# Performance work log

Hardware: AMD Instinct MI355X
Metric: run time of the kernel (lower is better)

Reference implementation:

```python
import jax, jax.numpy as jnp
import numpy as np

B, TY, TX, TT, H, VS, VT = 32, 64, 64, 64, 512, 32000, 32000


def setup_inputs() -> dict:
    key = jax.random.key(0)
    ks = jax.random.split(key, 12)
    s = 0.05  # weight scale for numerical sanity
    return {
        "y_hidden": jax.random.normal(ks[0], (B, TY, H), jnp.float32),
        "y_hidden_null": jax.random.normal(ks[1], (1, H), jnp.float32),
        "target_state": jax.random.normal(ks[2], (B, TT, H), jnp.float32),
        "W_em": jax.random.normal(ks[3], (H, H), jnp.float32) * s,
        "b_em": jnp.zeros((H,), jnp.float32),
        "W_sv": jax.random.normal(ks[4], (H, VS), jnp.float32) * s,
        "b_sv": jnp.zeros((VS,), jnp.float32),
        "W_tv": jax.random.normal(ks[5], (H, VT), jnp.float32) * s,
        "b_tv": jnp.zeros((VT,), jnp.float32),
        "sources": jax.random.randint(ks[6], (B, TX), 0, VS, jnp.int32),
        "targets": jax.random.randint(ks[7], (B, TT), 0, VT, jnp.int32),
        "target_lengths": jax.random.randint(ks[8], (B,), 1, TT + 1, jnp.int32),
    }


def reference(y_hidden, y_hidden_null, target_state, W_em, b_em, W_sv, b_sv,
              W_tv, b_tv, sources, targets, target_lengths):
    # ---- emission (get_emission) ----
    ts = jnp.tanh(y_hidden @ W_em + b_em)            # (B, Ty, H)
    tsn = jnp.tanh(y_hidden_null @ W_em + b_em)      # (1, H)
    em_sm = jax.nn.softmax(ts @ W_sv + b_sv, axis=-1)        # (B, Ty, Vs)
    null_sm = jax.nn.softmax(tsn @ W_sv + b_sv, axis=-1)     # (1, Vs)
    # vectorized replacement of tf.map_fn + tf.gather: per-batch gather of source token columns
    em_g = jnp.take_along_axis(em_sm, sources[:, None, :], axis=-1)  # (B, Ty, Tx)
    null_g = null_sm[0][sources]                                     # (B, Tx)
    null_tiled = jnp.broadcast_to(null_g[:, None, :], (sources.shape[0], ts.shape[1], sources.shape[1]))
    emission_prob = jnp.concatenate([em_g, null_tiled], axis=1)      # (B, 2*Ty, Tx)

    # ---- reconstruction (get_target); keep_prob = 1 so dropout is identity ----
    tgt_sm = jax.nn.softmax(target_state @ W_tv + b_tv, axis=-1)     # (B, Tt, Vt)
    target_predicted = jnp.argmax(tgt_sm, axis=-1)                   # (B, Tt)
    # gather[t, targets[t]] then * eye then reduce_sum == diagonal pick: prob of own token
    target_prob = jnp.take_along_axis(tgt_sm, targets[:, :, None].astype(jnp.int32), axis=-1)[..., 0]  # (B, Tt)
    Tt = targets.shape[1]
    target_mask = (jnp.arange(Tt)[None, :] < target_lengths[:, None]).astype(target_prob.dtype)
    reconstruction_expectation = target_prob * target_mask
    reconstruction_expectation_log = jnp.log(target_prob) * target_mask
    return emission_prob, reconstruction_expectation, reconstruction_expectation_log, target_predicted
```

## Files before the change

### kernel.cpp

```cpp
#include <hip/hip_runtime.h>
#include <math.h>

#define H 512
#define V 32000
#define NVB 250

typedef unsigned short ushort_t;
typedef __attribute__((ext_vector_type(8))) short short8;
typedef __attribute__((ext_vector_type(4))) float f32x4;

__device__ __forceinline__ unsigned short f2bf(float x) {
    unsigned int u; __builtin_memcpy(&u, &x, 4);
    unsigned int r = (u + 0x7fffu + ((u >> 16) & 1u)) >> 16;
    return (unsigned short)r;
}
__device__ __forceinline__ float bfu2f(unsigned short h) {
    unsigned int u = ((unsigned int)h) << 16;
    float f; __builtin_memcpy(&f, &u, 4);
    return f;
}

__device__ __forceinline__ void t2_insert(float& m1, int& c1, float& m2, int& c2,
                                          float v, int idx) {
    if (v > m1 || (v == m1 && idx < c1)) { m2 = m1; c2 = c1; m1 = v; c1 = idx; }
    else if (v > m2 || (v == m2 && idx < c2)) { m2 = v; c2 = idx; }
}

__device__ __forceinline__ void gl16(const void* g, void* l) {
    __builtin_amdgcn_global_load_lds(
        (const __attribute__((address_space(1))) void*)g,
        (__attribute__((address_space(3))) void*)l,
        16, 0, 0);
}

__global__ __launch_bounds__(256) void k_emstate(
    const float* __restrict__ y_hidden, const float* __restrict__ y_null,
    const float* __restrict__ W, const float* __restrict__ bias,
    float* __restrict__ ts)
{
    const int NR = 2049;
    __shared__ float As[16][64];
    __shared__ float Bs[16][64];
    int rb = blockIdx.y, cb = blockIdx.x;
    int row0 = rb * 64, col0 = cb * 64;
    int tid = threadIdx.x;
    int tr = tid >> 4, tc = tid & 15;
    float acc[4][4] = {};
    for (int k0 = 0; k0 < H; k0 += 16) {
        {
            int r = tid >> 2;
            int kk = (tid & 3) << 2;
            int row = row0 + r;
            float4 v = make_float4(0.f, 0.f, 0.f, 0.f);
            if (row < 2048)       v = *(const float4*)&y_hidden[row * H + k0 + kk];
            else if (row == 2048) v = *(const float4*)&y_null[k0 + kk];
            As[kk + 0][r] = v.x; As[kk + 1][r] = v.y;
            As[kk + 2][r] = v.z; As[kk + 3][r] = v.w;
            int bk = tid >> 4, bc = (tid & 15) << 2;
            *(float4*)&Bs[bk][bc] = *(const float4*)&W[(k0 + bk) * H + col0 + bc];
        }
        __syncthreads();
#pragma unroll
        for (int kk = 0; kk < 16; ++kk) {
            float4 a = *(float4*)&As[kk][tr * 4];
            float4 b = *(float4*)&Bs[kk][tc * 4];
            float av[4] = {a.x, a.y, a.z, a.w};
            float bv[4] = {b.x, b.y, b.z, b.w};
#pragma unroll
            for (int i = 0; i < 4; i++)
#pragma unroll
                for (int j = 0; j < 4; j++) acc[i][j] += av[i] * bv[j];
        }
        __syncthreads();
    }
#pragma unroll
    for (int i = 0; i < 4; i++) {
        int row = row0 + tr * 4 + i;
        if (row >= NR) break;
#pragma unroll
        for (int j = 0; j < 4; j++) {
            int col = col0 + tc * 4 + j;
            ts[(size_t)row * H + col] = tanhf(acc[i][j] + bias[col]);
        }
    }
}

__global__ __launch_bounds__(256) void k_packA(
    const float* __restrict__ A, int nvalid, int nb16,
    ushort_t* __restrict__ Ph, ushort_t* __restrict__ Pl)
{
    int c = blockIdx.x * 256 + threadIdx.x;
    if (c >= nb16 * 1024) return;
    int n16 = c >> 10, rem = c & 1023, k32 = rem >> 6, l = rem & 63;
    int m = n16 * 16 + (l & 15);
    int k = k32 * 32 + (l >> 4) * 8;
    float v[8];
    if (m < nvalid) {
        *(float4*)&v[0] = *(const float4*)&A[(size_t)m * H + k];
        *(float4*)&v[4] = *(const float4*)&A[(size_t)m * H + k + 4];
    } else {
#pragma unroll
        for (int j = 0; j < 8; ++j) v[j] = 0.f;
    }
    unsigned int hh[4], lo[4];
#pragma unroll
    for (int p = 0; p < 4; ++p) {
        unsigned short h0 = f2bf(v[2 * p]), h1 = f2bf(v[2 * p + 1]);
        hh[p] = (unsigned int)h0 | ((unsigned int)h1 << 16);
        unsigned short l0 = f2bf(v[2 * p] - bfu2f(h0));
        unsigned short l1 = f2bf(v[2 * p + 1] - bfu2f(h1));
        lo[p] = (unsigned int)l0 | ((unsigned int)l1 << 16);
    }
    size_t o = ((size_t)n16 * 16 + k32) * 512 + l * 8;
    *(uint4*)&Ph[o] = make_uint4(hh[0], hh[1], hh[2], hh[3]);
    *(uint4*)&Pl[o] = make_uint4(lo[0], lo[1], lo[2], lo[3]);
}

__global__ __launch_bounds__(256) void k_packW(
    const float* __restrict__ W,
    ushort_t* __restrict__ Ph, ushort_t* __restrict__ Pl)
{
    int c = blockIdx.x * 256 + threadIdx.x;
    int n16 = c >> 10, rem = c & 1023, k32 = rem >> 6, l = rem & 63;
    int n = n16 * 16 + (l & 15);
    int k = k32 * 32 + (l >> 4) * 8;
    float v[8];
#pragma unroll
    for (int j = 0; j < 8; ++j) v[j] = W[(size_t)(k + j) * V + n];
    unsigned int hh[4], lo[4];
#pragma unroll
    for (int p = 0; p < 4; ++p) {
        unsigned short h0 = f2bf(v[2 * p]), h1 = f2bf(v[2 * p + 1]);
        hh[p] = (unsigned int)h0 | ((unsigned int)h1 << 16);
        unsigned short l0 = f2bf(v[2 * p] - bfu2f(h0));
        unsigned short l1 = f2bf(v[2 * p + 1] - bfu2f(h1));
        lo[p] = (unsigned int)l0 | ((unsigned int)l1 << 16);
    }
    size_t o = ((size_t)n16 * 16 + k32) * 512 + l * 8;
    *(uint4*)&Ph[o] = make_uint4(hh[0], hh[1], hh[2], hh[3]);
    *(uint4*)&Pl[o] = make_uint4(lo[0], lo[1], lo[2], lo[3]);
}

template<bool TOP2>
__global__ __launch_bounds__(256, 1) void k_gemm(
    const ushort_t* __restrict__ Ah, const ushort_t* __restrict__ Al,
    const ushort_t* __restrict__ Bh, const ushort_t* __restrict__ Bl,
    const float* __restrict__ bias,
    float* __restrict__ pL,
    float* __restrict__ pM1, float* __restrict__ pM2,
    int* __restrict__ pI1, int* __restrict__ pI2)
{
    __shared__ __attribute__((aligned(16))) ushort_t Ash[8 * 512];
    __shared__ __attribute__((aligned(16))) ushort_t Asl[8 * 512];
    __shared__ __attribute__((aligned(16))) ushort_t Bsh[8 * 512];
    __shared__ __attribute__((aligned(16))) ushort_t Bsl[8 * 512];
    __shared__ float sc_s[128][2];
    __shared__ float sc_m1[128][2], sc_m2[128][2];
    __shared__ int   sc_c1[128][2], sc_c2[128][2];

    const int tid = threadIdx.x;
    const int vb = blockIdx.x, rb = blockIdx.y;
    const int row0 = rb * 128, col0 = vb * 128;
    const int lane = tid & 63, w = tid >> 6;
    const int wy = w >> 1, wx = w & 1;

    f32x4 acc[4][4];
#pragma unroll
    for (int i = 0; i < 4; ++i)
#pragma unroll
        for (int j = 0; j < 4; ++j)
#pragma unroll
            for (int r = 0; r < 4; ++r) acc[i][j][r] = 0.f;

    const ushort_t* gsrc = (w == 0) ? Ah : (w == 1) ? Al : (w == 2) ? Bh : Bl;
    ushort_t* ldst = (w == 0) ? Ash : (w == 1) ? Asl : (w == 2) ? Bsh : Bsl;
    const int n16base = ((w < 2) ? row0 : col0) >> 4;

    for (int it = 0; it < 16; ++it) {
        __syncthreads();
#pragma unroll
        for (int mb = 0; mb < 8; ++mb)
            gl16(gsrc + (((size_t)(n16base + mb) * 16 + it) << 9) + lane * 8,
                 ldst + mb * 512);
        __syncthreads();

        short8 ahf[4], alf[4], bhf[4], blf[4];
#pragma unroll
        for (int i = 0; i < 4; ++i) {
            ahf[i] = *(const short8*)&Ash[((wy * 4 + i) << 9) + (lane << 3)];
            alf[i] = *(const short8*)&Asl[((wy * 4 + i) << 9) + (lane << 3)];
            bhf[i] = *(const short8*)&Bsh[((wx * 4 + i) << 9) + (lane << 3)];
            blf[i] = *(const short8*)&Bsl[((wx * 4 + i) << 9) + (lane << 3)];
        }
#pragma unroll
        for (int i = 0; i < 4; ++i)
#pragma unroll
            for (int j = 0; j < 4; ++j) {
                acc[i][j] = __builtin_amdgcn_mfma_f32_16x16x32_bf16(ahf[i], bhf[j], acc[i][j], 0, 0, 0);
                acc[i][j] = __builtin_amdgcn_mfma_f32_16x16x32_bf16(ahf[i], blf[j], acc[i][j], 0, 0, 0);
                acc[i][j] = __builtin_amdgcn_mfma_f32_16x16x32_bf16(alf[i], bhf[j], acc[i][j], 0, 0, 0);
            }
    }

    float b4[4];
#pragma unroll
    for (int j = 0; j < 4; ++j) b4[j] = bias[col0 + wx * 64 + j * 16 + (lane & 15)];
    const int colbase = col0 + wx * 64 + (lane & 15);

#pragma unroll
    for (int i = 0; i < 4; ++i) {
#pragma unroll
        for (int r = 0; r < 4; ++r) {
            float s = 0.f;
            float m1 = -3e38f, m2 = -3e38f; int c1 = 0x7fffffff, c2 = 0x7fffffff;
#pragma unroll
            for (int j = 0; j < 4; ++j) {
                float v = acc[i][j][r] + b4[j];
                s += __expf(v);
                if (TOP2) t2_insert(m1, c1, m2, c2, v, colbase + j * 16);
            }
            for (int st = 1; st < 16; st <<= 1) {
                s += __shfl_xor(s, st, 64);
                if (TOP2) {
                    float om1 = __shfl_xor(m1, st, 64); int oc1 = __shfl_xor(c1, st, 64);
                    float om2 = __shfl_xor(m2, st, 64); int oc2 = __shfl_xor(c2, st, 64);
                    t2_insert(m1, c1, m2, c2, om1, oc1);
                    t2_insert(m1, c1, m2, c2, om2, oc2);
                }
            }
            if ((lane & 15) == 0) {
                int rowLoc = wy * 64 + i * 16 + (lane >> 4) * 4 + r;
                sc_s[rowLoc][wx] = s;
                if (TOP2) {
                    sc_m1[rowLoc][wx] = m1; sc_c1[rowLoc][wx] = c1;
                    sc_m2[rowLoc][wx] = m2; sc_c2[rowLoc][wx] = c2;
                }
            }
        }
    }
    __syncthreads();
    if (tid < 128) {
        int rowG = row0 + tid;
        pL[(size_t)rowG * NVB + vb] = sc_s[tid][0] + sc_s[tid][1];
        if (TOP2) {
            float m1 = sc_m1[tid][0]; int c1 = sc_c1[tid][0];
            float m2 = sc_m2[tid][0]; int c2 = sc_c2[tid][0];
            t2_insert(m1, c1, m2, c2, sc_m1[tid][1], sc_c1[tid][1]);
            t2_insert(m1, c1, m2, c2, sc_m2[tid][1], sc_c2[tid][1]);
            pM1[(size_t)rowG * NVB + vb] = m1;
            pM2[(size_t)rowG * NVB + vb] = m2;
            pI1[(size_t)rowG * NVB + vb] = c1;
            pI2[(size_t)rowG * NVB + vb] = c2;
        }
    }
}

__global__ __launch_bounds__(256) void k_combine_src(
    const float* __restrict__ pL, int nrows, float* __restrict__ L)
{
    int w = threadIdx.x >> 6, ll = threadIdx.x & 63;
    int row = blockIdx.x * 4 + w;
    if (row >= nrows) return;
    const float* p = &pL[(size_t)row * NVB];
    float s = 0.f;
    for (int vb = ll; vb < NVB; vb += 64) s += p[vb];
    for (int st = 1; st < 64; st <<= 1) s += __shfl_xor(s, st, 64);
    if (ll == 0) L[row] = s;
}

__global__ __launch_bounds__(256) void k_combine_tgt(
    const float* __restrict__ pL,
    const float* __restrict__ pM1, const float* __restrict__ pM2,
    const int* __restrict__ pI1, const int* __restrict__ pI2,
    float* __restrict__ L, int* __restrict__ C0, int* __restrict__ C1)
{
    int w = threadIdx.x >> 6, ll = threadIdx.x & 63;
    int row = blockIdx.x * 4 + w;
    if (row >= 2048) return;
    size_t base = (size_t)row * NVB;
    float s = 0.f;
    float m1 = -3e38f, m2 = -3e38f; int c1 = 0x7fffffff, c2 = 0x7fffffff;
    for (int vb = ll; vb < NVB; vb += 64) {
        s += pL[base + vb];
        t2_insert(m1, c1, m2, c2, pM1[base + vb], pI1[base + vb]);
        t2_insert(m1, c1, m2, c2, pM2[base + vb], pI2[base + vb]);
    }
    for (int st = 1; st < 64; st <<= 1) {
        s += __shfl_xor(s, st, 64);
        float om1 = __shfl_xor(m1, st, 64); int oc1 = __shfl_xor(c1, st, 64);
        float om2 = __shfl_xor(m2, st, 64); int oc2 = __shfl_xor(c2, st, 64);
        t2_insert(m1, c1, m2, c2, om1, oc1);
        t2_insert(m1, c1, m2, c2, om2, oc2);
    }
    if (ll == 0) { L[row] = s; C0[row] = c1; C1[row] = c2; }
}

__global__ __launch_bounds__(256) void k_emission(
    const float* __restrict__ ts, const float* __restrict__ W_sv,
    const float* __restrict__ b_sv, const int* __restrict__ sources,
    const float* __restrict__ L, float* __restrict__ out)
{
    __shared__ float wcol[H];
    __shared__ float sbias;
    int b = blockIdx.y, tx = blockIdx.x;
    int tid = threadIdx.x;
    int s = sources[b * 64 + tx];
    wcol[tid]       = W_sv[(size_t)tid * V + s];
    wcol[tid + 256] = W_sv[(size_t)(tid + 256) * V + s];
    if (tid == 0) sbias = b_sv[s];
    __syncthreads();
    int w = tid >> 6, ll = tid & 63;
    for (int r = w; r <= 64; r += 4) {
        int row = (r < 64) ? (b * 64 + r) : 2048;
        const float* a = &ts[(size_t)row * H];
        float sum = 0.f;
#pragma unroll
        for (int j = 0; j < 8; ++j) sum += a[ll * 8 + j] * wcol[ll * 8 + j];
        for (int m2 = 1; m2 < 64; m2 <<= 1) sum += __shfl_xor(sum, m2, 64);
        float prob = __expf(sum + sbias) / L[row];
        if (r < 64) {
            if (ll == 0) out[b * 8192 + r * 64 + tx] = prob;
        } else {
            out[b * 8192 + (64 + ll) * 64 + tx] = prob;
        }
    }
}

__global__ __launch_bounds__(256) void k_target_final(
    const float* __restrict__ tstate,
    const float* __restrict__ W_tv, const float* __restrict__ b_tv,
    const int* __restrict__ targets, const int* __restrict__ tlen,
    const float* __restrict__ L, const int* __restrict__ C0,
    const int* __restrict__ C1,
    float* __restrict__ out_exp, float* __restrict__ out_log,
    float* __restrict__ out_pred)
{
    int w = threadIdx.x >> 6, ll = threadIdx.x & 63;
    int row = blockIdx.x * 4 + w;
    if (row >= 2048) return;
    int tok = targets[row], a0 = C0[row], a1 = C1[row];
    const float* a = &tstate[(size_t)row * H];
    float s0 = 0.f, s1 = 0.f, s2 = 0.f;
#pragma unroll
    for (int j = 0; j < 8; ++j) {
        int k = ll * 8 + j;
        float av = a[k];
        const float* wr = &W_tv[(size_t)k * V];
        s0 += av * wr[tok]; s1 += av * wr[a0]; s2 += av * wr[a1];
    }
    for (int st = 1; st < 64; st <<= 1) {
        s0 += __shfl_xor(s0, st, 64);
        s1 += __shfl_xor(s1, st, 64);
        s2 += __shfl_xor(s2, st, 64);
    }
    if (ll == 0) {
        float ltok = s0 + b_tv[tok];
        float v0 = s1 + b_tv[a0], v1 = s2 + b_tv[a1];
        int pred = (v1 > v0 || (v1 == v0 && a1 < a0)) ? a1 : a0;
        float Li = L[row];
        int bb = row >> 6, t = row & 63;
        int mask = (t < tlen[bb]) ? 1 : 0;
        float prob = __expf(ltok) / Li;
        out_exp[row]  = mask ? prob : 0.f;
        out_log[row]  = mask ? (ltok - __logf(Li)) : 0.f;
        out_pred[row] = (float)pred;
    }
}

extern "C" void kernel_launch(void* const* d_in, const int* in_sizes, int n_in,
                              void* d_out, int out_size, void* d_ws, size_t ws_size,
                              hipStream_t stream)
{
    const float* y_hidden = (const float*)d_in[0];
    const float* y_null   = (const float*)d_in[1];
    const float* tstate   = (const float*)d_in[2];
    const float* W_em     = (const float*)d_in[3];
    const float* b_em     = (const float*)d_in[4];
    const float* W_sv     = (const float*)d_in[5];
    const float* b_sv     = (const float*)d_in[6];
    const float* W_tv     = (const float*)d_in[7];
    const float* b_tv     = (const float*)d_in[8];
    const int*   sources  = (const int*)d_in[9];
    const int*   targets  = (const int*)d_in[10];
    const int*   tlen     = (const int*)d_in[11];

    float* out = (float*)d_out;
    float* out_em   = out;
    float* out_exp  = out + 262144;
    float* out_log  = out + 264192;
    float* out_pred = out + 266240;

    float* ws = (float*)d_ws;
    size_t off = 0;
    float*    ts    = ws + off; off += (size_t)2176 * H;
    ushort_t* tsPh  = (ushort_t*)(ws + off); off += (size_t)2176 * H / 2;
    ushort_t* tsPl  = (ushort_t*)(ws + off); off += (size_t)2176 * H / 2;
    ushort_t* ttPh  = (ushort_t*)(ws + off); off += (size_t)2048 * H / 2;
    ushort_t* ttPl  = (ushort_t*)(ws + off); off += (size_t)2048 * H / 2;
    ushort_t* Wh    = (ushort_t*)(ws + off); off += (size_t)V * H / 2;
    ushort_t* Wl    = (ushort_t*)(ws + off); off += (size_t)V * H / 2;
    float* pL0  = ws + off; off += (size_t)2176 * NVB;
    float* pL1  = ws + off; off += (size_t)2048 * NVB;
    float* pM1a = ws + off; off += (size_t)2048 * NVB;
    float* pM1b = ws + off; off += (size_t)2048 * NVB;
    int*   pI1a = (int*)(ws + off); off += (size_t)2048 * NVB;
    int*   pI1b = (int*)(ws + off); off += (size_t)2048 * NVB;
    float* L0   = ws + off; off += 2176;
    float* L1   = ws + off; off += 2048;
    int*   C0   = (int*)(ws + off); off += 2048;
    int*   C1   = (int*)(ws + off); off += 2048;

    k_emstate<<<dim3(8, 33), 256, 0, stream>>>(y_hidden, y_null, W_em, b_em, ts);

    k_packA<<<(136 * 1024) / 256, 256, 0, stream>>>(ts, 2049, 136, tsPh, tsPl);
    k_packA<<<(128 * 1024) / 256, 256, 0, stream>>>(tstate, 2048, 128, ttPh, ttPl);

    k_packW<<<(2000 * 1024) / 256, 256, 0, stream>>>(W_sv, Wh, Wl);
    k_gemm<false><<<dim3(NVB, 17), 256, 0, stream>>>(
        tsPh, tsPl, Wh, Wl, b_sv, pL0, nullptr, nullptr, nullptr, nullptr);

    k_packW<<<(2000 * 1024) / 256, 256, 0, stream>>>(W_tv, Wh, Wl);
    k_gemm<true><<<dim3(NVB, 16), 256, 0, stream>>>(
        ttPh, ttPl, Wh, Wl, b_tv, pL1, pM1a, pM1b, pI1a, pI1b);

    k_combine_src<<<(2049 + 3) / 4, 256, 0, stream>>>(pL0, 2049, L0);
    k_combine_tgt<<<2048 / 4, 256, 0, stream>>>(pL1, pM1a, pM1b, pI1a, pI1b,
                                                L1, C0, C1);

    k_emission<<<dim3(64, 32), 256, 0, stream>>>(ts, W_sv, b_sv, sources, L0, out_em);

    k_target_final<<<2048 / 4, 256, 0, stream>>>(tstate, W_tv, b_tv, targets, tlen,
                                                 L1, C0, C1,
                                                 out_exp, out_log, out_pred);
}
```

Measured before the change: 1.381 ms.

## Load GEMM fragments directly from global into registers with double buffering

```diff
diff --git a/kernel.cpp b/kernel.cpp
--- a/kernel.cpp
+++ b/kernel.cpp
@@ -24,13 +24,6 @@
                                           float v, int idx) {
     if (v > m1 || (v == m1 && idx < c1)) { m2 = m1; c2 = c1; m1 = v; c1 = idx; }
     else if (v > m2 || (v == m2 && idx < c2)) { m2 = v; c2 = idx; }
-}
-
-__device__ __forceinline__ void gl16(const void* g, void* l) {
-    __builtin_amdgcn_global_load_lds(
-        (const __attribute__((address_space(1))) void*)g,
-        (__attribute__((address_space(3))) void*)l,
-        16, 0, 0);
 }
 
 __global__ __launch_bounds__(256) void k_emstate(
@@ -142,7 +135,7 @@
 }
 
 template<bool TOP2>
-__global__ __launch_bounds__(256, 1) void k_gemm(
+__global__ __launch_bounds__(256) void k_gemm(
     const ushort_t* __restrict__ Ah, const ushort_t* __restrict__ Al,
     const ushort_t* __restrict__ Bh, const ushort_t* __restrict__ Bl,
     const float* __restrict__ bias,
@@ -150,16 +143,12 @@
     float* __restrict__ pM1, float* __restrict__ pM2,
     int* __restrict__ pI1, int* __restrict__ pI2)
 {
-    __shared__ __attribute__((aligned(16))) ushort_t Ash[8 * 512];
-    __shared__ __attribute__((aligned(16))) ushort_t Asl[8 * 512];
-    __shared__ __attribute__((aligned(16))) ushort_t Bsh[8 * 512];
-    __shared__ __attribute__((aligned(16))) ushort_t Bsl[8 * 512];
     __shared__ float sc_s[128][2];
     __shared__ float sc_m1[128][2], sc_m2[128][2];
     __shared__ int   sc_c1[128][2], sc_c2[128][2];
 
     const int tid = threadIdx.x;
-    const int vb = blockIdx.x, rb = blockIdx.y;
+    const int rb = blockIdx.x, vb = blockIdx.y;
     const int row0 = rb * 128, col0 = vb * 128;
     const int lane = tid & 63, w = tid >> 6;
     const int wy = w >> 1, wx = w & 1;
@@ -172,35 +161,53 @@
 #pragma unroll
             for (int r = 0; r < 4; ++r) acc[i][j][r] = 0.f;
 
-    const ushort_t* gsrc = (w == 0) ? Ah : (w == 1) ? Al : (w == 2) ? Bh : Bl;
-    ushort_t* ldst = (w == 0) ? Ash : (w == 1) ? Asl : (w == 2) ? Bsh : Bsl;
-    const int n16base = ((w < 2) ? row0 : col0) >> 4;
-
-    for (int it = 0; it < 16; ++it) {
-        __syncthreads();
-#pragma unroll
-        for (int mb = 0; mb < 8; ++mb)
-            gl16(gsrc + (((size_t)(n16base + mb) * 16 + it) << 9) + lane * 8,
-                 ldst + mb * 512);
-        __syncthreads();
-
-        short8 ahf[4], alf[4], bhf[4], blf[4];
-#pragma unroll
-        for (int i = 0; i < 4; ++i) {
-            ahf[i] = *(const short8*)&Ash[((wy * 4 + i) << 9) + (lane << 3)];
-            alf[i] = *(const short8*)&Asl[((wy * 4 + i) << 9) + (lane << 3)];
-            bhf[i] = *(const short8*)&Bsh[((wx * 4 + i) << 9) + (lane << 3)];
-            blf[i] = *(const short8*)&Bsl[((wx * 4 + i) << 9) + (lane << 3)];
-        }
-#pragma unroll
-        for (int i = 0; i < 4; ++i)
-#pragma unroll
-            for (int j = 0; j < 4; ++j) {
-                acc[i][j] = __builtin_amdgcn_mfma_f32_16x16x32_bf16(ahf[i], bhf[j], acc[i][j], 0, 0, 0);
-                acc[i][j] = __builtin_amdgcn_mfma_f32_16x16x32_bf16(ahf[i], blf[j], acc[i][j], 0, 0, 0);
-                acc[i][j] = __builtin_amdgcn_mfma_f32_16x16x32_bf16(alf[i], bhf[j], acc[i][j], 0, 0, 0);
-            }
-    }
+    const int nA = (row0 >> 4) + wy * 4;
+    const int nB = (col0 >> 4) + wx * 4;
+    const ushort_t* aH = Ah + (size_t)nA * 8192 + lane * 8;
+    const ushort_t* aL = Al + (size_t)nA * 8192 + lane * 8;
+    const ushort_t* bH = Bh + (size_t)nB * 8192 + lane * 8;
+    const ushort_t* bL = Bl + (size_t)nB * 8192 + lane * 8;
+
+    short8 a0h[4], a0l[4], b0h[4], b0l[4];
+    short8 a1h[4], a1l[4], b1h[4], b1l[4];
+
+#define LOAD_ITER(AH, AL, BH, BL, it)                                   \
+    {                                                                   \
+        const size_t ko = (size_t)(it) * 512;                           \
+        _Pragma("unroll")                                               \
+        for (int i = 0; i < 4; ++i) {                                   \
+            AH[i] = *(const short8*)(aH + (size_t)i * 8192 + ko);       \
+            AL[i] = *(const short8*)(aL + (size_t)i * 8192 + ko);       \
+            BH[i] = *(const short8*)(bH + (size_t)i * 8192 + ko);       \
+            BL[i] = *(const short8*)(bL + (size_t)i * 8192 + ko);       \
+        }                                                               \
+    }
+
+#define COMP_ITER(AH, AL, BH, BL)                                       \
+    {                                                                   \
+        _Pragma("unroll")                                               \
+        for (int i = 0; i < 4; ++i)                                     \
+            _Pragma("unroll")                                           \
+            for (int j = 0; j < 4; ++j) {                               \
+                acc[i][j] = __builtin_amdgcn_mfma_f32_16x16x32_bf16(    \
+                    AH[i], BH[j], acc[i][j], 0, 0, 0);                  \
+                acc[i][j] = __builtin_amdgcn_mfma_f32_16x16x32_bf16(    \
+                    AH[i], BL[j], acc[i][j], 0, 0, 0);                  \
+                acc[i][j] = __builtin_amdgcn_mfma_f32_16x16x32_bf16(    \
+                    AL[i], BH[j], acc[i][j], 0, 0, 0);                  \
+            }                                                           \
+    }
+
+    LOAD_ITER(a0h, a0l, b0h, b0l, 0)
+#pragma unroll
+    for (int it = 0; it < 16; it += 2) {
+        if (it + 1 < 16) LOAD_ITER(a1h, a1l, b1h, b1l, it + 1)
+        COMP_ITER(a0h, a0l, b0h, b0l)
+        if (it + 2 < 16) LOAD_ITER(a0h, a0l, b0h, b0l, it + 2)
+        if (it + 1 < 16) COMP_ITER(a1h, a1l, b1h, b1l)
+    }
+#undef LOAD_ITER
+#undef COMP_ITER
 
     float b4[4];
 #pragma unroll
@@ -416,11 +423,11 @@
     k_packA<<<(128 * 1024) / 256, 256, 0, stream>>>(tstate, 2048, 128, ttPh, ttPl);
 
     k_packW<<<(2000 * 1024) / 256, 256, 0, stream>>>(W_sv, Wh, Wl);
-    k_gemm<false><<<dim3(NVB, 17), 256, 0, stream>>>(
+    k_gemm<false><<<dim3(17, NVB), 256, 0, stream>>>(
         tsPh, tsPl, Wh, Wl, b_sv, pL0, nullptr, nullptr, nullptr, nullptr);
 
     k_packW<<<(2000 * 1024) / 256, 256, 0, stream>>>(W_tv, Wh, Wl);
-    k_gemm<true><<<dim3(NVB, 16), 256, 0, stream>>>(
+    k_gemm<true><<<dim3(16, NVB), 256, 0, stream>>>(
         ttPh, ttPl, Wh, Wl, b_tv, pL1, pM1a, pM1b, pI1a, pI1b);
 
     k_combine_src<<<(2049 + 3) / 4, 256, 0, stream>>>(pL0, 2049, L0);
```

Result: slower. 1.591 ms (+15.3%).

## Double-buffer GEMM LDS tiles, swap grid order, relax launch bounds

Applied to the files above, without the earlier changes.

```diff
diff --git a/kernel.cpp b/kernel.cpp
--- a/kernel.cpp
+++ b/kernel.cpp
@@ -142,7 +142,7 @@
 }
 
 template<bool TOP2>
-__global__ __launch_bounds__(256, 1) void k_gemm(
+__global__ __launch_bounds__(256) void k_gemm(
     const ushort_t* __restrict__ Ah, const ushort_t* __restrict__ Al,
     const ushort_t* __restrict__ Bh, const ushort_t* __restrict__ Bl,
     const float* __restrict__ bias,
@@ -150,16 +150,16 @@
     float* __restrict__ pM1, float* __restrict__ pM2,
     int* __restrict__ pI1, int* __restrict__ pI2)
 {
-    __shared__ __attribute__((aligned(16))) ushort_t Ash[8 * 512];
-    __shared__ __attribute__((aligned(16))) ushort_t Asl[8 * 512];
-    __shared__ __attribute__((aligned(16))) ushort_t Bsh[8 * 512];
-    __shared__ __attribute__((aligned(16))) ushort_t Bsl[8 * 512];
+    __shared__ __attribute__((aligned(16))) ushort_t AshB[2][8 * 512];
+    __shared__ __attribute__((aligned(16))) ushort_t AslB[2][8 * 512];
+    __shared__ __attribute__((aligned(16))) ushort_t BshB[2][8 * 512];
+    __shared__ __attribute__((aligned(16))) ushort_t BslB[2][8 * 512];
     __shared__ float sc_s[128][2];
     __shared__ float sc_m1[128][2], sc_m2[128][2];
     __shared__ int   sc_c1[128][2], sc_c2[128][2];
 
     const int tid = threadIdx.x;
-    const int vb = blockIdx.x, rb = blockIdx.y;
+    const int rb = blockIdx.x, vb = blockIdx.y;
     const int row0 = rb * 128, col0 = vb * 128;
     const int lane = tid & 63, w = tid >> 6;
     const int wy = w >> 1, wx = w & 1;
@@ -173,24 +173,39 @@
             for (int r = 0; r < 4; ++r) acc[i][j][r] = 0.f;
 
     const ushort_t* gsrc = (w == 0) ? Ah : (w == 1) ? Al : (w == 2) ? Bh : Bl;
-    ushort_t* ldst = (w == 0) ? Ash : (w == 1) ? Asl : (w == 2) ? Bsh : Bsl;
+    ushort_t* ld0 = (w == 0) ? AshB[0] : (w == 1) ? AslB[0] : (w == 2) ? BshB[0] : BslB[0];
+    ushort_t* ld1 = (w == 0) ? AshB[1] : (w == 1) ? AslB[1] : (w == 2) ? BshB[1] : BslB[1];
     const int n16base = ((w < 2) ? row0 : col0) >> 4;
 
+#pragma unroll
+    for (int mb = 0; mb < 8; ++mb)
+        gl16(gsrc + (((size_t)(n16base + mb) * 16 + 0) << 9) + lane * 8,
+             ld0 + mb * 512);
+
+#pragma unroll 2
     for (int it = 0; it < 16; ++it) {
-        __syncthreads();
-#pragma unroll
-        for (int mb = 0; mb < 8; ++mb)
-            gl16(gsrc + (((size_t)(n16base + mb) * 16 + it) << 9) + lane * 8,
-                 ldst + mb * 512);
-        __syncthreads();
+        const int cur = it & 1;
+        __builtin_amdgcn_s_waitcnt(0x0F70);
+        __builtin_amdgcn_s_barrier();
+        if (it < 15) {
+            ushort_t* nxt = cur ? ld0 : ld1;
+#pragma unroll
+            for (int mb = 0; mb < 8; ++mb)
+                gl16(gsrc + (((size_t)(n16base + mb) * 16 + (it + 1)) << 9) + lane * 8,
+                     nxt + mb * 512);
+        }
+        const ushort_t* cAh = AshB[cur];
+        const ushort_t* cAl = AslB[cur];
+        const ushort_t* cBh = BshB[cur];
+        const ushort_t* cBl = BslB[cur];
 
         short8 ahf[4], alf[4], bhf[4], blf[4];
 #pragma unroll
         for (int i = 0; i < 4; ++i) {
-            ahf[i] = *(const short8*)&Ash[((wy * 4 + i) << 9) + (lane << 3)];
-            alf[i] = *(const short8*)&Asl[((wy * 4 + i) << 9) + (lane << 3)];
-            bhf[i] = *(const short8*)&Bsh[((wx * 4 + i) << 9) + (lane << 3)];
-            blf[i] = *(const short8*)&Bsl[((wx * 4 + i) << 9) + (lane << 3)];
+            ahf[i] = *(const short8*)&cAh[((wy * 4 + i) << 9) + (lane << 3)];
+            alf[i] = *(const short8*)&cAl[((wy * 4 + i) << 9) + (lane << 3)];
+            bhf[i] = *(const short8*)&cBh[((wx * 4 + i) << 9) + (lane << 3)];
+            blf[i] = *(const short8*)&cBl[((wx * 4 + i) << 9) + (lane << 3)];
         }
 #pragma unroll
         for (int i = 0; i < 4; ++i)
@@ -416,11 +431,11 @@
     k_packA<<<(128 * 1024) / 256, 256, 0, stream>>>(tstate, 2048, 128, ttPh, ttPl);
 
     k_packW<<<(2000 * 1024) / 256, 256, 0, stream>>>(W_sv, Wh, Wl);
-    k_gemm<false><<<dim3(NVB, 17), 256, 0, stream>>>(
+    k_gemm<false><<<dim3(17, NVB), 256, 0, stream>>>(
         tsPh, tsPl, Wh, Wl, b_sv, pL0, nullptr, nullptr, nullptr, nullptr);
 
     k_packW<<<(2000 * 1024) / 256, 256, 0, stream>>>(W_tv, Wh, Wl);
-    k_gemm<true><<<dim3(NVB, 16), 256, 0, stream>>>(
+    k_gemm<true><<<dim3(16, NVB), 256, 0, stream>>>(
         ttPh, ttPl, Wh, Wl, b_tv, pL1, pM1a, pM1b, pI1a, pI1b);
 
     k_combine_src<<<(2049 + 3) / 4, 256, 0, stream>>>(pL0, 2049, L0);
```

New measurement: 1.375 ms. No clear change (-0.4%).
